# Kernel optimization log

Hardware: AMD Instinct MI355X
Metric: run time of the kernel (lower is better)

Reference implementation:

```python
import jax, jax.numpy as jnp
import numpy as np

EPS = 1e-12
BN_EPS = 1e-5

LAP = jnp.array([[0., 1., 0.], [1., -4., 1.], [0., 1., 0.]], jnp.float32).reshape(1, 1, 3, 3)
SOBX = jnp.array([[-1., 0., 1.], [-2., 0., 2.], [-1., 0., 1.]], jnp.float32).reshape(1, 1, 3, 3)
SOBY = jnp.array([[-1., -2., -1.], [0., 0., 0.], [1., 2., 1.]], jnp.float32).reshape(1, 1, 3, 3)


def _conv3x3(x, w):
    return jax.lax.conv_general_dilated(x, w, (1, 1), 'SAME',
                                        dimension_numbers=('NCHW', 'OIHW', 'NCHW'))


def _bn(x, gamma, beta, mean, var):
    # eval-mode BatchNorm2d with running stats
    inv = gamma / jnp.sqrt(var + BN_EPS)
    return x * inv[None, :, None, None] + (beta - mean * inv)[None, :, None, None]


def _entropy_u8(x01, bins=256):
    # torch.histc(min=0,max=1): bin i = [i/bins,(i+1)/bins), value==1 -> last bin
    B = x01.shape[0]
    flat = jnp.clip(x01, 0.0, 1.0).reshape(B, -1)
    idx = jnp.clip(jnp.floor(flat * bins).astype(jnp.int32), 0, bins - 1)
    h = jnp.zeros((B, bins), flat.dtype).at[jnp.arange(B)[:, None], idx].add(1.0)
    p = h / (h.sum(axis=1, keepdims=True) + EPS)
    safe_p = jnp.where(p > 0, p, 1.0)
    return jnp.where(p > 0, -p * jnp.log2(safe_p), 0.0).sum(axis=1)


def _gini(flat):
    B, N = flat.shape
    xs = jnp.sort(flat, axis=1)
    s = xs.sum(axis=1) + EPS
    w = (N + 1 - jnp.arange(1, N + 1, dtype=flat.dtype))[None, :]
    lor = (w * xs).sum(axis=1) / s
    return (N + 1 - 2.0 * lor) / N


def _grid_cv(E, grid=16):
    B, _, H, W = E.shape  # H,W divisible by grid -> adaptive_avg_pool == block mean
    pooled = E.reshape(B, grid, H // grid, grid, W // grid).mean(axis=(2, 4))
    cells = pooled.reshape(B, -1)
    return cells.std(axis=1) / (cells.mean(axis=1) + EPS)


def _lap_var(x):
    y = _conv3x3(x, LAP)
    return jnp.var(y, axis=(2, 3), ddof=1)[:, 0]  # torch .var default unbiased=True


def _sobel_mean(x):
    gx = _conv3x3(x, SOBX)
    gy = _conv3x3(x, SOBY)
    return jnp.sqrt(gx * gx + gy * gy).mean(axis=(1, 2, 3))


def _colorfulness(R, G, Bc):
    rg = (R - G)[:, 0]
    yb = ((R + G) / 2 - Bc)[:, 0]
    # torch .std default is unbiased (ddof=1)
    s = jnp.sqrt(jnp.std(rg, axis=(1, 2), ddof=1) ** 2 + jnp.std(yb, axis=(1, 2), ddof=1) ** 2)
    m = jnp.sqrt(rg.mean(axis=(1, 2)) ** 2 + yb.mean(axis=(1, 2)) ** 2)
    return s + 0.3 * m


def _metrics(img5):
    B = img5.shape[0]
    P, N = img5[:, 0:1], img5[:, 1:2]
    R, G, Bc = img5[:, 2:3], img5[:, 3:4], img5[:, 4:5]
    Pn, Nn = P / 255.0, N / 255.0
    E = jnp.maximum(Pn + Nn, 0.0)
    Y = jnp.clip(0.299 * R + 0.587 * G + 0.114 * Bc, 0.0, 1.0)
    muY = Y.mean(axis=(1, 2, 3))
    stdY = Y.std(axis=(1, 2, 3))  # unbiased=False
    flatY = Y.reshape(B, -1)
    dr = jnp.quantile(flatY, 0.99, axis=1) - jnp.quantile(flatY, 0.01, axis=1)
    psat = (Y < 0.02).astype(Y.dtype).mean(axis=(1, 2, 3)) + (Y > 0.98).astype(Y.dtype).mean(axis=(1, 2, 3))
    entY = _entropy_u8(Y)
    varlp = _lap_var(Y)
    gmean = _sobel_mean(Y)
    cf = _colorfulness(R, G, Bc)
    nz = (E > 0).astype(E.dtype).mean(axis=(1, 2, 3))
    int_density = E.mean(axis=(1, 2, 3))
    onoff = (Pn.sum(axis=(1, 2, 3)) + EPS) / (Nn.sum(axis=(1, 2, 3)) + EPS)
    gg = _gini(E.reshape(B, -1))
    cvgrid = _grid_cv(E)
    entE = _entropy_u8(E)
    varlpE = _lap_var(E)
    pbias = ((Pn - Nn) / (Pn + Nn + EPS)).mean(axis=(1, 2, 3))
    z16 = jnp.stack([muY, stdY, dr, psat, entY, varlp, gmean, cf, nz, int_density,
                     onoff, gg, cvgrid, entE, varlpE, pbias], axis=1)
    return z16[:, jnp.array([0, 1, 5, 6, 12, 9, 15, 14])]


def _forward(event, frame, conv1_w, bn1_g, bn1_b, bn1_m, bn1_v,
             conv2_w, bn2_g, bn2_b, bn2_m, bn2_v,
             fe_w1, fe_b1, fe_w2, fe_b2, hg_w, hg_b, hf_w, hf_b, res_scale):
    img5 = jnp.concatenate([event, frame], axis=1)  # (B,5,H,W)
    fx = _conv3x3(img5, conv1_w)
    fx = _bn(fx, bn1_g, bn1_b, bn1_m, bn1_v)
    fx = fx * jax.nn.sigmoid(fx)  # SiLU
    fx = _conv3x3(fx, conv2_w)
    fx = _bn(fx, bn2_g, bn2_b, bn2_m, bn2_v)
    z = jax.lax.stop_gradient(_metrics(img5))  # @torch.no_grad()
    h = jax.nn.relu(z @ fe_w1.T + fe_b1)
    h = jax.nn.relu(h @ fe_w2.T + fe_b2)
    g = jax.nn.sigmoid(h @ hg_w.T + hg_b)
    g = g / (g.sum(axis=1, keepdims=True) + EPS)
    film = h @ hf_w.T + hf_b  # (B,10)
    gamma = 1.0 + 0.1 * film[:, :5]
    beta = 0.1 * film[:, 5:]
    fx_film = gamma[:, :, None, None] * fx + beta[:, :, None, None]
    alpha = jnp.concatenate([jnp.repeat(g[:, 0:1], 2, axis=1),
                             jnp.repeat(g[:, 1:2], 3, axis=1)], axis=1)
    fused = fx_film * alpha[:, :, None, None]
    out5 = img5 + res_scale[0] * fused
    return out5


def setup_inputs() -> dict:
    key = jax.random.key(0)
    ks = jax.random.split(key, 21)
    B, H, W = 16, 512, 512
    CH, HID, MD = 16, 64, 8
    u = lambda k, s, off=0.0: jax.random.uniform(k, s, jnp.float32) + off
    n = lambda k, s, sc=0.1: jax.random.normal(k, s, jnp.float32) * sc
    return {
        'event': u(ks[0], (B, 2, H, W)),
        'frame': u(ks[1], (B, 3, H, W)),
        'conv1_w': n(ks[2], (CH, 5, 3, 3)),
        'bn1_g': u(ks[3], (CH,), 0.5), 'bn1_b': n(ks[4], (CH,)),
        'bn1_m': n(ks[5], (CH,)), 'bn1_v': u(ks[6], (CH,), 0.5),
        'conv2_w': n(ks[7], (5, CH, 3, 3)),
        'bn2_g': u(ks[8], (5,), 0.5), 'bn2_b': n(ks[9], (5,)),
        'bn2_m': n(ks[10], (5,)), 'bn2_v': u(ks[11], (5,), 0.5),
        'fe_w1': n(ks[12], (HID, MD)), 'fe_b1': n(ks[13], (HID,)),
        'fe_w2': n(ks[14], (HID, HID)), 'fe_b2': n(ks[15], (HID,)),
        'hg_w': n(ks[16], (2, HID)), 'hg_b': n(ks[17], (2,)),
        'hf_w': n(ks[18], (10, HID)), 'hf_b': n(ks[19], (10,)),
        'res_scale': n(ks[20], (1,)),
    }


def reference(event, frame, conv1_w, bn1_g, bn1_b, bn1_m, bn1_v,
              conv2_w, bn2_g, bn2_b, bn2_m, bn2_v,
              fe_w1, fe_b1, fe_w2, fe_b2, hg_w, hg_b, hf_w, hf_b, res_scale):
    out5 = _forward(event, frame, conv1_w, bn1_g, bn1_b, bn1_m, bn1_v,
                    conv2_w, bn2_g, bn2_b, bn2_m, bn2_v,
                    fe_w1, fe_b1, fe_w2, fe_b2, hg_w, hg_b, hf_w, hf_b, res_scale)
    return out5[:, 0:2], out5[:, 2:5]
```

## Files before the change

### kernel.cpp

```cpp
#include <hip/hip_runtime.h>
#include <hip/hip_bf16.h>

typedef unsigned int   u32;
typedef unsigned short u16;

#define HW 262144
#define W512 512

typedef __attribute__((ext_vector_type(8))) short short8;
typedef __attribute__((ext_vector_type(4))) float f32x4;

__device__ __forceinline__ u32 f2b_rtne(float f) {
    union { float f; u32 i; } c; c.f = f;
    u32 u = c.i;
    return (u + 0x7FFFu + ((u >> 16) & 1u)) >> 16;
}
__device__ __forceinline__ u32 pk_bf16(float lo, float hi) {
    float2 t; t.x = lo; t.y = hi;
    __hip_bfloat162 h = __float22bfloat162_rn(t);
    return *reinterpret_cast<u32*>(&h);
}
__device__ __forceinline__ float lo16(u32 w) {
    union { u32 i; float f; } c; c.i = w << 16; return c.f;
}
__device__ __forceinline__ float hi16(u32 w) {
    union { u32 i; float f; } c; c.i = w & 0xFFFF0000u; return c.f;
}
__device__ __forceinline__ float silu_fast(float v) {
    return v * __builtin_amdgcn_rcpf(1.f + __expf(-v));
}

__device__ __forceinline__ void row6(const u16* rowp, int base, float* o) {
    uint2 A = *reinterpret_cast<const uint2*>(rowp + base - 4);
    uint2 B = *reinterpret_cast<const uint2*>(rowp + base);
    uint2 C = *reinterpret_cast<const uint2*>(rowp + base + 4);
    o[0] = hi16(A.y);
    o[1] = lo16(B.x); o[2] = hi16(B.x);
    o[3] = lo16(B.y); o[4] = hi16(B.y);
    o[5] = lo16(C.x);
}

__global__ __launch_bounds__(1024) void k_band(
    const float* __restrict__ ev, const float* __restrict__ fr,
    int nb, float* __restrict__ partials, float* __restrict__ z)
{
    __shared__ u16 sYb[18][528];
    __shared__ u16 sEb[18][528];
    __shared__ float cellPart[1024];
    __shared__ float cellFull[256];
    __shared__ float red[16][8];

    int blk = blockIdx.x;
    int b = blk / nb, band = blk % nb;
    int rowsPerBand = 512 / nb;
    int chunks = rowsPerBand >> 4;
    int rBase = band * rowsPerBand;
    int tid = threadIdx.x;

    const float* Pp = ev + (size_t)(b * 2)     * HW;
    const float* Np = ev + (size_t)(b * 2 + 1) * HW;
    const float* Rp = fr + (size_t)(b * 3)     * HW;
    const float* Gp = fr + (size_t)(b * 3 + 1) * HW;
    const float* Bp = fr + (size_t)(b * 3 + 2) * HW;

    if (nb == 1 && tid < 256) cellFull[tid] = 0.f;
    if (tid < 36) {
        int rr = tid >> 1, side = tid & 1;
        uint4 zz = {0, 0, 0, 0};
        *reinterpret_cast<uint4*>(&sYb[rr][side ? 520 : 0]) = zz;
        *reinterpret_cast<uint4*>(&sEb[rr][side ? 520 : 0]) = zz;
    }

    float aY = 0, aY2 = 0, aL = 0, aL2 = 0, aG = 0, aPb = 0, aLE = 0, aLE2 = 0;

    for (int ch = 0; ch < chunks; ++ch) {
        int r0 = rBase + ch * 16;
        __syncthreads();
        for (int idx = tid; idx < 2304; idx += 1024) {
            int rl = idx >> 7, q4 = (idx & 127) << 2;
            int gy = r0 - 1 + rl;
            float4 y4 = {0.f, 0.f, 0.f, 0.f};
            float4 e4 = {0.f, 0.f, 0.f, 0.f};
            if (gy >= 0 && gy < W512) {
                size_t o = (size_t)gy * W512 + q4;
                float4 R = *reinterpret_cast<const float4*>(Rp + o);
                float4 G = *reinterpret_cast<const float4*>(Gp + o);
                float4 B = *reinterpret_cast<const float4*>(Bp + o);
                float4 P = *reinterpret_cast<const float4*>(Pp + o);
                float4 N = *reinterpret_cast<const float4*>(Np + o);
                y4.x = fminf(fmaxf(0.299f * R.x + 0.587f * G.x + 0.114f * B.x, 0.f), 1.f);
                y4.y = fminf(fmaxf(0.299f * R.y + 0.587f * G.y + 0.114f * B.y, 0.f), 1.f);
                y4.z = fminf(fmaxf(0.299f * R.z + 0.587f * G.z + 0.114f * B.z, 0.f), 1.f);
                y4.w = fminf(fmaxf(0.299f * R.w + 0.587f * G.w + 0.114f * B.w, 0.f), 1.f);
                e4.x = fmaxf((P.x + N.x) * (1.f / 255.f), 0.f);
                e4.y = fmaxf((P.y + N.y) * (1.f / 255.f), 0.f);
                e4.z = fmaxf((P.z + N.z) * (1.f / 255.f), 0.f);
                e4.w = fmaxf((P.w + N.w) * (1.f / 255.f), 0.f);
                if (rl >= 1 && rl <= 16) {
                    float pnx = P.x * (1.f / 255.f), nnx = N.x * (1.f / 255.f);
                    float pny = P.y * (1.f / 255.f), nny = N.y * (1.f / 255.f);
                    float pnz = P.z * (1.f / 255.f), nnz = N.z * (1.f / 255.f);
                    float pnw = P.w * (1.f / 255.f), nnw = N.w * (1.f / 255.f);
                    aPb += (pnx - nnx) * __builtin_amdgcn_rcpf(pnx + nnx + 1e-12f);
                    aPb += (pny - nny) * __builtin_amdgcn_rcpf(pny + nny + 1e-12f);
                    aPb += (pnz - nnz) * __builtin_amdgcn_rcpf(pnz + nnz + 1e-12f);
                    aPb += (pnw - nnw) * __builtin_amdgcn_rcpf(pnw + nnw + 1e-12f);
                }
            }
            uint2 py, pe;
            py.x = pk_bf16(y4.x, y4.y); py.y = pk_bf16(y4.z, y4.w);
            pe.x = pk_bf16(e4.x, e4.y); pe.y = pk_bf16(e4.z, e4.w);
            *reinterpret_cast<uint2*>(&sYb[rl][8 + q4]) = py;
            *reinterpret_cast<uint2*>(&sEb[rl][8 + q4]) = pe;
        }
        __syncthreads();

        float ce = 0.f;
        #pragma unroll
        for (int q = 0; q < 2; ++q) {
            int qi = tid + (q << 10);
            int row = qi >> 7, c4 = (qi & 127) << 2;
            int lr = row + 1, base = 8 + c4;
            float y0[6], y1[6], y2[6], er[6];
            row6(&sYb[lr - 1][0], base, y0);
            row6(&sYb[lr][0],     base, y1);
            row6(&sYb[lr + 1][0], base, y2);
            row6(&sEb[lr][0],     base, er);
            uint2 U = *reinterpret_cast<const uint2*>(&sEb[lr - 1][base]);
            uint2 D = *reinterpret_cast<const uint2*>(&sEb[lr + 1][base]);
            float eu[4] = {lo16(U.x), hi16(U.x), lo16(U.y), hi16(U.y)};
            float ed[4] = {lo16(D.x), hi16(D.x), lo16(D.y), hi16(D.y)};
            #pragma unroll
            for (int j = 0; j < 4; ++j) {
                float y = y1[j + 1];
                float lap = y0[j + 1] + y2[j + 1] + y1[j] + y1[j + 2] - 4.f * y;
                float gx  = (y0[j + 2] + 2.f * y1[j + 2] + y2[j + 2])
                          - (y0[j]     + 2.f * y1[j]     + y2[j]);
                float gy2 = (y2[j] + 2.f * y2[j + 1] + y2[j + 2])
                          - (y0[j] + 2.f * y0[j + 1] + y0[j + 2]);
                float gm = sqrtf(gx * gx + gy2 * gy2);
                float e = er[j + 1];
                float lapE = eu[j] + ed[j] + er[j] + er[j + 2] - 4.f * e;
                aY += y; aY2 += y * y; aL += lap; aL2 += lap * lap; aG += gm;
                aLE += lapE; aLE2 += lapE * lapE; ce += e;
            }
        }
        cellPart[tid] = ce;
        __syncthreads();
        if (tid < 16) {
            float s = 0.f;
            for (int rg = 0; rg < 8; ++rg)
                for (int k = 0; k < 8; ++k)
                    s += cellPart[rg * 128 + tid * 8 + k];
            if (nb == 1) cellFull[(r0 >> 5) * 16 + tid] += s;
            else         partials[(size_t)blk * 32 + 9 + tid] = s;
        }
    }
    __syncthreads();

    float v[8] = {aY, aY2, aL, aL2, aG, aPb, aLE, aLE2};
    #pragma unroll
    for (int off = 32; off; off >>= 1)
        #pragma unroll
        for (int k = 0; k < 8; ++k) v[k] += __shfl_down(v[k], off);
    int lane = tid & 63, wid = tid >> 6;
    if (lane == 0)
        for (int k = 0; k < 8; ++k) red[wid][k] = v[k];
    __syncthreads();

    if (tid == 0) {
        float s[8];
        for (int k = 0; k < 8; ++k) {
            float t = 0.f;
            for (int w = 0; w < 16; ++w) t += red[w][k];
            s[k] = t;
        }
        if (nb > 1) {
            float* rec = partials + (size_t)blk * 32;
            for (int k = 0; k < 8; ++k) rec[k] = s[k];
        } else {
            float c1 = 0.f, c2 = 0.f, ct = 0.f;
            for (int j = 0; j < 256; ++j) {
                float m = cellFull[j] * (1.f / 1024.f);
                c1 += m; c2 += m * m; ct += cellFull[j];
            }
            const float FN = 262144.f;
            float muY   = s[0] / FN;
            float stdY  = sqrtf(fmaxf(s[1] / FN - muY * muY, 0.f));
            float varlp = fmaxf(s[3] - s[2] * s[2] / FN, 0.f) / (FN - 1.f);
            float gmean = s[4] / FN;
            float mc = c1 * (1.f / 256.f);
            float vc = fmaxf(c2 * (1.f / 256.f) - mc * mc, 0.f);
            float cv = sqrtf(vc) / (mc + 1e-12f);
            float dens = ct / FN;
            float pb = s[5] / FN;
            float varlpE = fmaxf(s[7] - s[6] * s[6] / FN, 0.f) / (FN - 1.f);
            float* zb = z + b * 8;
            zb[0] = muY; zb[1] = stdY; zb[2] = varlp; zb[3] = gmean;
            zb[4] = cv;  zb[5] = dens; zb[6] = pb;    zb[7] = varlpE;
        }
    }
}

__global__ __launch_bounds__(256) void k_finalize(
    const float* __restrict__ partials, float* __restrict__ z)
{
    __shared__ float sred[8];
    __shared__ float rr[4][3];
    int b = blockIdx.x, tid = threadIdx.x;
    if (tid < 8) {
        float s = 0.f;
        for (int band = 0; band < 32; ++band)
            s += partials[(size_t)(b * 32 + band) * 32 + tid];
        sred[tid] = s;
    }
    int cr = tid >> 4, cc = tid & 15;
    float cell = partials[(size_t)(b * 32 + 2 * cr)     * 32 + 9 + cc]
               + partials[(size_t)(b * 32 + 2 * cr + 1) * 32 + 9 + cc];
    float m = cell * (1.f / 1024.f);
    float c1 = m, c2 = m * m, ct = cell;
    #pragma unroll
    for (int off = 32; off; off >>= 1) {
        c1 += __shfl_down(c1, off);
        c2 += __shfl_down(c2, off);
        ct += __shfl_down(ct, off);
    }
    int lane = tid & 63, wid = tid >> 6;
    if (lane == 0) { rr[wid][0] = c1; rr[wid][1] = c2; rr[wid][2] = ct; }
    __syncthreads();
    if (tid == 0) {
        float C1 = rr[0][0] + rr[1][0] + rr[2][0] + rr[3][0];
        float C2 = rr[0][1] + rr[1][1] + rr[2][1] + rr[3][1];
        float CT = rr[0][2] + rr[1][2] + rr[2][2] + rr[3][2];
        const float FN = 262144.f;
        float muY   = sred[0] / FN;
        float stdY  = sqrtf(fmaxf(sred[1] / FN - muY * muY, 0.f));
        float varlp = fmaxf(sred[3] - sred[2] * sred[2] / FN, 0.f) / (FN - 1.f);
        float gmean = sred[4] / FN;
        float mc = C1 * (1.f / 256.f);
        float vc = fmaxf(C2 * (1.f / 256.f) - mc * mc, 0.f);
        float cv = sqrtf(vc) / (mc + 1e-12f);
        float dens = CT / FN;
        float pb = sred[5] / FN;
        float varlpE = fmaxf(sred[7] - sred[6] * sred[6] / FN, 0.f) / (FN - 1.f);
        float* zb = z + b * 8;
        zb[0] = muY; zb[1] = stdY; zb[2] = varlp; zb[3] = gmean;
        zb[4] = cv;  zb[5] = dens; zb[6] = pb;    zb[7] = varlpE;
    }
}

__global__ __launch_bounds__(1024) void k_mlp(
    const float* __restrict__ z,
    const float* __restrict__ w1, const float* __restrict__ b1,
    const float* __restrict__ w2, const float* __restrict__ b2,
    const float* __restrict__ hgw, const float* __restrict__ hgb,
    const float* __restrict__ hfw, const float* __restrict__ hfb,
    const float* __restrict__ rs,
    const float* __restrict__ c1w,
    const float* __restrict__ bn1g, const float* __restrict__ bn1b,
    const float* __restrict__ bn1m, const float* __restrict__ bn1v,
    const float* __restrict__ c2w,
    const float* __restrict__ bn2g, const float* __restrict__ bn2b,
    const float* __restrict__ bn2m, const float* __restrict__ bn2v,
    float* __restrict__ coefA, float* __restrict__ cBp,
    u16* __restrict__ w1frag, u16* __restrict__ w2frag,
    float* __restrict__ b1f)
{
    int j = threadIdx.x, b = threadIdx.y;
    int ft = b * 64 + j;

    for (int t = ft; t < 1536; t += 1024) {
        int m = t >> 9, ln = (t >> 3) & 63, sl = t & 7;
        int oc = ln & 15, gg = ln >> 4;
        int tap = m * 4 + gg;
        float v = 0.f;
        if (tap < 9 && sl < 5)
            v = c1w[oc * 45 + sl * 9 + tap] * (bn1g[oc] * rsqrtf(bn1v[oc] + 1e-5f));
        w1frag[t] = (u16)f2b_rtne(v);
    }
    for (int t = ft; t < 2560; t += 1024) {
        int m = t >> 9, ln = (t >> 3) & 63, sl = t & 7;
        int oc = ln & 15, gg = ln >> 4;
        int tap = 2 * m + (gg >> 1);
        int ic = (gg & 1) * 8 + sl;
        float v = 0.f;
        if (oc < 5 && tap < 9)
            v = c2w[oc * 144 + ic * 9 + tap] * (bn2g[oc] * rsqrtf(bn2v[oc] + 1e-5f));
        w2frag[t] = (u16)f2b_rtne(v);
    }
    if (ft < 16) {
        float inv = bn1g[ft] * rsqrtf(bn1v[ft] + 1e-5f);
        b1f[ft] = bn1b[ft] - bn1m[ft] * inv;
    }

    __shared__ float sZ[16][8], sH1[16][64], sH2[16][64], sG[16][2], sF[16][10];
    if (j < 8) sZ[b][j] = z[b * 8 + j];
    __syncthreads();
    float a = b1[j];
    #pragma unroll
    for (int k = 0; k < 8; ++k) a += sZ[b][k] * w1[j * 8 + k];
    sH1[b][j] = fmaxf(a, 0.f);
    __syncthreads();
    float a2 = b2[j];
    for (int k = 0; k < 64; ++k) a2 += sH1[b][k] * w2[j * 64 + k];
    sH2[b][j] = fmaxf(a2, 0.f);
    __syncthreads();
    if (j < 2) {
        float g = hgb[j];
        for (int k = 0; k < 64; ++k) g += sH2[b][k] * hgw[j * 64 + k];
        sG[b][j] = 1.f / (1.f + __expf(-g));
    }
    if (j < 10) {
        float f = hfb[j];
        for (int k = 0; k < 64; ++k) f += sH2[b][k] * hfw[j * 64 + k];
        sF[b][j] = f;
    }
    __syncthreads();
    if (j < 5) {
        float gs = sG[b][0] + sG[b][1] + 1e-12f;
        float alpha = (j < 2 ? sG[b][0] : sG[b][1]) / gs;
        float gamma = 1.f + 0.1f * sF[b][j];
        float beta  = 0.1f * sF[b][5 + j];
        float r = rs[0];
        float inv2 = bn2g[j] * rsqrtf(bn2v[j] + 1e-5f);
        float b2fold = bn2b[j] - bn2m[j] * inv2;
        float cA = r * alpha * gamma;
        coefA[b * 5 + j] = cA;
        cBp[b * 5 + j]   = r * alpha * beta + cA * b2fold;
    }
}

__global__ __launch_bounds__(256, 4) void k_main(
    const float* __restrict__ ev, const float* __restrict__ fr,
    const u16* __restrict__ w1frag, const u16* __restrict__ w2frag,
    const float* __restrict__ b1f,
    const float* __restrict__ coefA, const float* __restrict__ cBp,
    float* __restrict__ out)
{
    __shared__ __align__(16) u16 sIn[20 * 40 * 8];
    __shared__ __align__(16) u16 sT1[18 * 34 * 16];

    int tid = threadIdx.x;
    int lane = tid & 63, wv = tid >> 6;
    int g = lane >> 4, col = lane & 15;
    int b = blockIdx.z;
    int ty0 = blockIdx.y * 16, tx0 = blockIdx.x * 32;
    bool interior = (blockIdx.x >= 1 && blockIdx.x <= 14 &&
                     blockIdx.y >= 1 && blockIdx.y <= 30);

    const float* p0 = ev + (size_t)(b * 2)     * HW;
    const float* p1 = ev + (size_t)(b * 2 + 1) * HW;
    const float* p2 = fr + (size_t)(b * 3)     * HW;
    const float* p3 = fr + (size_t)(b * 3 + 1) * HW;
    const float* p4 = fr + (size_t)(b * 3 + 2) * HW;

    if (tid < 200) {
        int r = tid / 10, k = tid % 10;
        int gy = ty0 - 2 + r, gx = tx0 - 4 + 4 * k;
        float4 v0, v1, v2, v3, v4;
        if (interior) {
            size_t o = (size_t)gy * W512 + gx;
            v0 = *reinterpret_cast<const float4*>(p0 + o);
            v1 = *reinterpret_cast<const float4*>(p1 + o);
            v2 = *reinterpret_cast<const float4*>(p2 + o);
            v3 = *reinterpret_cast<const float4*>(p3 + o);
            v4 = *reinterpret_cast<const float4*>(p4 + o);
        } else {
            v0 = v1 = v2 = v3 = v4 = float4{0, 0, 0, 0};
            if (gy >= 0 && gy < W512 && gx >= 0 && gx < W512) {
                size_t o = (size_t)gy * W512 + gx;
                v0 = *reinterpret_cast<const float4*>(p0 + o);
                v1 = *reinterpret_cast<const float4*>(p1 + o);
                v2 = *reinterpret_cast<const float4*>(p2 + o);
                v3 = *reinterpret_cast<const float4*>(p3 + o);
                v4 = *reinterpret_cast<const float4*>(p4 + o);
            }
        }
        int base = (r * 40 + 4 * k) * 8;
        const float* a0 = (const float*)&v0;
        const float* a1 = (const float*)&v1;
        const float* a2 = (const float*)&v2;
        const float* a3 = (const float*)&v3;
        const float* a4 = (const float*)&v4;
        #pragma unroll
        for (int jx = 0; jx < 4; ++jx) {
            uint4 pk;
            pk.x = pk_bf16(a0[jx], a1[jx]);
            pk.y = pk_bf16(a2[jx], a3[jx]);
            pk.z = pk_bf16(a4[jx], 0.f);
            pk.w = 0;
            *reinterpret_cast<uint4*>(&sIn[base + jx * 8]) = pk;
        }
    }

    short8 a1f[3], a2f[5];
    #pragma unroll
    for (int m = 0; m < 3; ++m)
        a1f[m] = *reinterpret_cast<const short8*>(&w1frag[(m * 64 + lane) * 8]);
    #pragma unroll
    for (int m = 0; m < 5; ++m)
        a2f[m] = *reinterpret_cast<const short8*>(&w2frag[(m * 64 + lane) * 8]);
    f32x4 b1v = *reinterpret_cast<const f32x4*>(&b1f[g * 4]);

    int boff1[3];
    #pragma unroll
    for (int m = 0; m < 3; ++m) {
        int tap = m * 4 + g; if (tap > 8) tap = 8;
        boff1[m] = ((tap / 3) * 40 + (tap % 3)) * 16;
    }
    int boff2[5];
    #pragma unroll
    for (int m = 0; m < 5; ++m) {
        int tap = 2 * m + (g >> 1); if (tap > 8) tap = 8;
        boff2[m] = ((tap / 3) * 34 + (tap % 3)) * 32 + (g & 1) * 16;
    }

    __syncthreads();

    for (int t = wv; t < 39; t += 8) {
        bool hasB = (t + 4 < 39);
        int qA = t * 16 + col;
        int qB = hasB ? (qA + 64) : qA;
        int qcA = qA > 611 ? 611 : qA;
        int qcB = qB > 611 ? 611 : qB;
        int rA = qcA / 34, cA = qcA - rA * 34;
        int rB = qcB / 34, cB = qcB - rB * 34;
        const char* baseA = (const char*)&sIn[(rA * 40 + cA + 2) * 8];
        const char* baseB = (const char*)&sIn[(rB * 40 + cB + 2) * 8];
        short8 fA0 = *reinterpret_cast<const short8*>(baseA + boff1[0]);
        short8 fB0 = *reinterpret_cast<const short8*>(baseB + boff1[0]);
        short8 fA1 = *reinterpret_cast<const short8*>(baseA + boff1[1]);
        short8 fB1 = *reinterpret_cast<const short8*>(baseB + boff1[1]);
        short8 fA2 = *reinterpret_cast<const short8*>(baseA + boff1[2]);
        short8 fB2 = *reinterpret_cast<const short8*>(baseB + boff1[2]);
        f32x4 accA = b1v;
        f32x4 accB = b1v;
        accA = __builtin_amdgcn_mfma_f32_16x16x32_bf16(a1f[0], fA0, accA, 0, 0, 0);
        accB = __builtin_amdgcn_mfma_f32_16x16x32_bf16(a1f[0], fB0, accB, 0, 0, 0);
        accA = __builtin_amdgcn_mfma_f32_16x16x32_bf16(a1f[1], fA1, accA, 0, 0, 0);
        accB = __builtin_amdgcn_mfma_f32_16x16x32_bf16(a1f[1], fB1, accB, 0, 0, 0);
        accA = __builtin_amdgcn_mfma_f32_16x16x32_bf16(a1f[2], fA2, accA, 0, 0, 0);
        accB = __builtin_amdgcn_mfma_f32_16x16x32_bf16(a1f[2], fB2, accB, 0, 0, 0);

        {
            float v0 = silu_fast(accA[0]);
            float v1 = silu_fast(accA[1]);
            float v2 = silu_fast(accA[2]);
            float v3 = silu_fast(accA[3]);
            if (!interior) {
                int gy1 = ty0 - 1 + rA, gx1 = tx0 - 1 + cA;
                bool inimg = (gy1 >= 0 && gy1 < W512 && gx1 >= 0 && gx1 < W512);
                if (!inimg) { v0 = v1 = v2 = v3 = 0.f; }
            }
            uint2 pk;
            pk.x = pk_bf16(v0, v1);
            pk.y = pk_bf16(v2, v3);
            *reinterpret_cast<uint2*>(&sT1[(rA * 34 + cA) * 16 + g * 4]) = pk;
        }
        if (hasB) {
            float v0 = silu_fast(accB[0]);
            float v1 = silu_fast(accB[1]);
            float v2 = silu_fast(accB[2]);
            float v3 = silu_fast(accB[3]);
            if (!interior) {
                int gy1 = ty0 - 1 + rB, gx1 = tx0 - 1 + cB;
                bool inimg = (gy1 >= 0 && gy1 < W512 && gx1 >= 0 && gx1 < W512);
                if (!inimg) { v0 = v1 = v2 = v3 = 0.f; }
            }
            uint2 pk;
            pk.x = pk_bf16(v0, v1);
            pk.y = pk_bf16(v2, v3);
            *reinterpret_cast<uint2*>(&sT1[(rB * 34 + cB) * 16 + g * 4]) = pk;
        }
    }
    __syncthreads();

    float cA0 = coefA[b * 5 + 0], cA1 = coefA[b * 5 + 1], cA2 = coefA[b * 5 + 2];
    float cA3 = coefA[b * 5 + 3], cA4 = coefA[b * 5 + 4];
    float cB0 = cBp[b * 5 + 0], cB1 = cBp[b * 5 + 1], cB2 = cBp[b * 5 + 2];
    float cB3 = cBp[b * 5 + 3], cB4 = cBp[b * 5 + 4];
    const size_t OUT2 = (size_t)32 * HW;

    for (int t = wv; t < 32; t += 8) {
        int qA = t * 16 + col;
        int qB = qA + 64;
        int rA = qA >> 5, cA = qA & 31;
        int rB = qB >> 5, cB = qB & 31;
        const char* baseA = (const char*)&sT1[(rA * 34 + cA) * 16];
        const char* baseB = (const char*)&sT1[(rB * 34 + cB) * 16];
        f32x4 accA = {0.f, 0.f, 0.f, 0.f};
        f32x4 accB = {0.f, 0.f, 0.f, 0.f};
        #pragma unroll
        for (int m = 0; m < 5; ++m) {
            short8 fA = *reinterpret_cast<const short8*>(baseA + boff2[m]);
            short8 fB = *reinterpret_cast<const short8*>(baseB + boff2[m]);
            accA = __builtin_amdgcn_mfma_f32_16x16x32_bf16(a2f[m], fA, accA, 0, 0, 0);
            accB = __builtin_amdgcn_mfma_f32_16x16x32_bf16(a2f[m], fB, accB, 0, 0, 0);
        }
        size_t pxA = (size_t)(ty0 + rA) * W512 + (tx0 + cA);
        size_t pxB = (size_t)(ty0 + rB) * W512 + (tx0 + cB);
        if (g == 0) {
            out[(size_t)(b * 2 + 0) * HW + pxA] = p0[pxA] + cA0 * accA[0] + cB0;
            out[(size_t)(b * 2 + 0) * HW + pxB] = p0[pxB] + cA0 * accB[0] + cB0;
            out[(size_t)(b * 2 + 1) * HW + pxA] = p1[pxA] + cA1 * accA[1] + cB1;
            out[(size_t)(b * 2 + 1) * HW + pxB] = p1[pxB] + cA1 * accB[1] + cB1;
            out[OUT2 + (size_t)(b * 3 + 0) * HW + pxA] = p2[pxA] + cA2 * accA[2] + cB2;
            out[OUT2 + (size_t)(b * 3 + 0) * HW + pxB] = p2[pxB] + cA2 * accB[2] + cB2;
            out[OUT2 + (size_t)(b * 3 + 1) * HW + pxA] = p3[pxA] + cA3 * accA[3] + cB3;
            out[OUT2 + (size_t)(b * 3 + 1) * HW + pxB] = p3[pxB] + cA3 * accB[3] + cB3;
        } else if (g == 1) {
            out[OUT2 + (size_t)(b * 3 + 2) * HW + pxA] = p4[pxA] + cA4 * accA[0] + cB4;
            out[OUT2 + (size_t)(b * 3 + 2) * HW + pxB] = p4[pxB] + cA4 * accB[0] + cB4;
        }
    }
}

extern "C" void kernel_launch(void* const* d_in, const int* in_sizes, int n_in,
                              void* d_out, int out_size, void* d_ws, size_t ws_size,
                              hipStream_t stream)
{
    const float* ev = (const float*)d_in[0];
    const float* fr = (const float*)d_in[1];

    char* wb = (char*)d_ws;
    float* coefA    = (float*)(wb + 0);
    float* cBp      = (float*)(wb + 320);
    float* b1f      = (float*)(wb + 640);
    u16*   w1frag   = (u16*) (wb + 768);
    u16*   w2frag   = (u16*) (wb + 3840);
    float* zbuf     = (float*)(wb + 8960);
    float* partials = (float*)(wb + 10240);

    bool fast = (ws_size >= 75776);
    int nb   = fast ? 32 : 1;
    int nblk = fast ? 512 : 16;
    k_band<<<dim3(nblk), dim3(1024), 0, stream>>>(ev, fr, nb, partials, zbuf);
    if (fast) k_finalize<<<dim3(16), dim3(256), 0, stream>>>(partials, zbuf);

    k_mlp<<<dim3(1), dim3(64, 16), 0, stream>>>(zbuf,
        (const float*)d_in[12], (const float*)d_in[13], (const float*)d_in[14], (const float*)d_in[15],
        (const float*)d_in[16], (const float*)d_in[17], (const float*)d_in[18], (const float*)d_in[19],
        (const float*)d_in[20],
        (const float*)d_in[2], (const float*)d_in[3], (const float*)d_in[4], (const float*)d_in[5],
        (const float*)d_in[6], (const float*)d_in[7], (const float*)d_in[8], (const float*)d_in[9],
        (const float*)d_in[10], (const float*)d_in[11],
        coefA, cBp, w1frag, w2frag, b1f);

    k_main<<<dim3(16, 32, 16), dim3(256), 0, stream>>>(ev, fr,
        w1frag, w2frag, b1f, coefA, cBp, (float*)d_out);
}
```

Measured before the change: 128.8 us.

## Fold finalize into MLP kernel, widen band stencil per thread, raise k_main occupancy

```diff
diff --git a/kernel.cpp b/kernel.cpp
--- a/kernel.cpp
+++ b/kernel.cpp
@@ -30,14 +30,16 @@
     return v * __builtin_amdgcn_rcpf(1.f + __expf(-v));
 }
 
-__device__ __forceinline__ void row6(const u16* rowp, int base, float* o) {
+__device__ __forceinline__ void unp10(const u16* rowp, int base, float* v) {
     uint2 A = *reinterpret_cast<const uint2*>(rowp + base - 4);
-    uint2 B = *reinterpret_cast<const uint2*>(rowp + base);
-    uint2 C = *reinterpret_cast<const uint2*>(rowp + base + 4);
-    o[0] = hi16(A.y);
-    o[1] = lo16(B.x); o[2] = hi16(B.x);
-    o[3] = lo16(B.y); o[4] = hi16(B.y);
-    o[5] = lo16(C.x);
+    uint4 B = *reinterpret_cast<const uint4*>(rowp + base);
+    uint2 C = *reinterpret_cast<const uint2*>(rowp + base + 8);
+    v[0] = hi16(A.y);
+    v[1] = lo16(B.x); v[2] = hi16(B.x);
+    v[3] = lo16(B.y); v[4] = hi16(B.y);
+    v[5] = lo16(B.z); v[6] = hi16(B.z);
+    v[7] = lo16(B.w); v[8] = hi16(B.w);
+    v[9] = lo16(C.x);
 }
 
 __global__ __launch_bounds__(1024) void k_band(
@@ -116,22 +118,23 @@
         __syncthreads();
 
         float ce = 0.f;
-        #pragma unroll
-        for (int q = 0; q < 2; ++q) {
-            int qi = tid + (q << 10);
-            int row = qi >> 7, c4 = (qi & 127) << 2;
-            int lr = row + 1, base = 8 + c4;
-            float y0[6], y1[6], y2[6], er[6];
-            row6(&sYb[lr - 1][0], base, y0);
-            row6(&sYb[lr][0],     base, y1);
-            row6(&sYb[lr + 1][0], base, y2);
-            row6(&sEb[lr][0],     base, er);
-            uint2 U = *reinterpret_cast<const uint2*>(&sEb[lr - 1][base]);
-            uint2 D = *reinterpret_cast<const uint2*>(&sEb[lr + 1][base]);
-            float eu[4] = {lo16(U.x), hi16(U.x), lo16(U.y), hi16(U.y)};
-            float ed[4] = {lo16(D.x), hi16(D.x), lo16(D.y), hi16(D.y)};
+        {
+            int row = tid >> 6;
+            int c8  = (tid & 63) << 3;
+            int lr = row + 1, base = 8 + c8;
+            float y0[10], y1[10], y2[10], er[10];
+            unp10(&sYb[lr - 1][0], base, y0);
+            unp10(&sYb[lr][0],     base, y1);
+            unp10(&sYb[lr + 1][0], base, y2);
+            unp10(&sEb[lr][0],     base, er);
+            uint4 U = *reinterpret_cast<const uint4*>(&sEb[lr - 1][base]);
+            uint4 D = *reinterpret_cast<const uint4*>(&sEb[lr + 1][base]);
+            float eu[8] = {lo16(U.x), hi16(U.x), lo16(U.y), hi16(U.y),
+                           lo16(U.z), hi16(U.z), lo16(U.w), hi16(U.w)};
+            float ed[8] = {lo16(D.x), hi16(D.x), lo16(D.y), hi16(D.y),
+                           lo16(D.z), hi16(D.z), lo16(D.w), hi16(D.w)};
             #pragma unroll
-            for (int j = 0; j < 4; ++j) {
+            for (int j = 0; j < 8; ++j) {
                 float y = y1[j + 1];
                 float lap = y0[j + 1] + y2[j + 1] + y1[j] + y1[j + 2] - 4.f * y;
                 float gx  = (y0[j + 2] + 2.f * y1[j + 2] + y2[j + 2])
@@ -149,9 +152,9 @@
         __syncthreads();
         if (tid < 16) {
             float s = 0.f;
-            for (int rg = 0; rg < 8; ++rg)
-                for (int k = 0; k < 8; ++k)
-                    s += cellPart[rg * 128 + tid * 8 + k];
+            for (int rg = 0; rg < 16; ++rg)
+                for (int k = 0; k < 4; ++k)
+                    s += cellPart[rg * 64 + tid * 4 + k];
             if (nb == 1) cellFull[(r0 >> 5) * 16 + tid] += s;
             else         partials[(size_t)blk * 32 + 9 + tid] = s;
         }
@@ -202,55 +205,8 @@
     }
 }
 
-__global__ __launch_bounds__(256) void k_finalize(
-    const float* __restrict__ partials, float* __restrict__ z)
-{
-    __shared__ float sred[8];
-    __shared__ float rr[4][3];
-    int b = blockIdx.x, tid = threadIdx.x;
-    if (tid < 8) {
-        float s = 0.f;
-        for (int band = 0; band < 32; ++band)
-            s += partials[(size_t)(b * 32 + band) * 32 + tid];
-        sred[tid] = s;
-    }
-    int cr = tid >> 4, cc = tid & 15;
-    float cell = partials[(size_t)(b * 32 + 2 * cr)     * 32 + 9 + cc]
-               + partials[(size_t)(b * 32 + 2 * cr + 1) * 32 + 9 + cc];
-    float m = cell * (1.f / 1024.f);
-    float c1 = m, c2 = m * m, ct = cell;
-    #pragma unroll
-    for (int off = 32; off; off >>= 1) {
-        c1 += __shfl_down(c1, off);
-        c2 += __shfl_down(c2, off);
-        ct += __shfl_down(ct, off);
-    }
-    int lane = tid & 63, wid = tid >> 6;
-    if (lane == 0) { rr[wid][0] = c1; rr[wid][1] = c2; rr[wid][2] = ct; }
-    __syncthreads();
-    if (tid == 0) {
-        float C1 = rr[0][0] + rr[1][0] + rr[2][0] + rr[3][0];
-        float C2 = rr[0][1] + rr[1][1] + rr[2][1] + rr[3][1];
-        float CT = rr[0][2] + rr[1][2] + rr[2][2] + rr[3][2];
-        const float FN = 262144.f;
-        float muY   = sred[0] / FN;
-        float stdY  = sqrtf(fmaxf(sred[1] / FN - muY * muY, 0.f));
-        float varlp = fmaxf(sred[3] - sred[2] * sred[2] / FN, 0.f) / (FN - 1.f);
-        float gmean = sred[4] / FN;
-        float mc = C1 * (1.f / 256.f);
-        float vc = fmaxf(C2 * (1.f / 256.f) - mc * mc, 0.f);
-        float cv = sqrtf(vc) / (mc + 1e-12f);
-        float dens = CT / FN;
-        float pb = sred[5] / FN;
-        float varlpE = fmaxf(sred[7] - sred[6] * sred[6] / FN, 0.f) / (FN - 1.f);
-        float* zb = z + b * 8;
-        zb[0] = muY; zb[1] = stdY; zb[2] = varlp; zb[3] = gmean;
-        zb[4] = cv;  zb[5] = dens; zb[6] = pb;    zb[7] = varlpE;
-    }
-}
-
 __global__ __launch_bounds__(1024) void k_mlp(
-    const float* __restrict__ z,
+    const float* __restrict__ zbuf, const float* __restrict__ partials, int fast,
     const float* __restrict__ w1, const float* __restrict__ b1,
     const float* __restrict__ w2, const float* __restrict__ b2,
     const float* __restrict__ hgw, const float* __restrict__ hgb,
@@ -293,9 +249,53 @@
         b1f[ft] = bn1b[ft] - bn1m[ft] * inv;
     }
 
-    __shared__ float sZ[16][8], sH1[16][64], sH2[16][64], sG[16][2], sF[16][10];
-    if (j < 8) sZ[b][j] = z[b * 8 + j];
-    __syncthreads();
+    __shared__ float sZ[16][8], sS[16][8], sH1[16][64], sH2[16][64], sG[16][2], sF[16][10];
+
+    if (fast) {
+        if (j < 8) {
+            float s = 0.f;
+            for (int band = 0; band < 32; ++band)
+                s += partials[(size_t)(b * 32 + band) * 32 + j];
+            sS[b][j] = s;
+        }
+        float c1 = 0.f, c2 = 0.f, ct = 0.f;
+        #pragma unroll
+        for (int k = 0; k < 4; ++k) {
+            int idx = j * 4 + k;
+            int cr = idx >> 4, cc = idx & 15;
+            float cell = partials[(size_t)(b * 32 + 2 * cr)     * 32 + 9 + cc]
+                       + partials[(size_t)(b * 32 + 2 * cr + 1) * 32 + 9 + cc];
+            float m = cell * (1.f / 1024.f);
+            c1 += m; c2 += m * m; ct += cell;
+        }
+        #pragma unroll
+        for (int off = 32; off; off >>= 1) {
+            c1 += __shfl_down(c1, off);
+            c2 += __shfl_down(c2, off);
+            ct += __shfl_down(ct, off);
+        }
+        __syncthreads();
+        if (j == 0) {
+            const float FN = 262144.f;
+            float muY   = sS[b][0] / FN;
+            float stdY  = sqrtf(fmaxf(sS[b][1] / FN - muY * muY, 0.f));
+            float varlp = fmaxf(sS[b][3] - sS[b][2] * sS[b][2] / FN, 0.f) / (FN - 1.f);
+            float gmean = sS[b][4] / FN;
+            float mc = c1 * (1.f / 256.f);
+            float vc = fmaxf(c2 * (1.f / 256.f) - mc * mc, 0.f);
+            float cv = sqrtf(vc) / (mc + 1e-12f);
+            float dens = ct / FN;
+            float pb = sS[b][5] / FN;
+            float varlpE = fmaxf(sS[b][7] - sS[b][6] * sS[b][6] / FN, 0.f) / (FN - 1.f);
+            sZ[b][0] = muY; sZ[b][1] = stdY; sZ[b][2] = varlp; sZ[b][3] = gmean;
+            sZ[b][4] = cv;  sZ[b][5] = dens; sZ[b][6] = pb;    sZ[b][7] = varlpE;
+        }
+        __syncthreads();
+    } else {
+        if (j < 8) sZ[b][j] = zbuf[b * 8 + j];
+        __syncthreads();
+    }
+
     float a = b1[j];
     #pragma unroll
     for (int k = 0; k < 8; ++k) a += sZ[b][k] * w1[j * 8 + k];
@@ -330,7 +330,7 @@
     }
 }
 
-__global__ __launch_bounds__(256, 4) void k_main(
+__global__ __launch_bounds__(256, 5) void k_main(
     const float* __restrict__ ev, const float* __restrict__ fr,
     const u16* __restrict__ w1frag, const u16* __restrict__ w2frag,
     const float* __restrict__ b1f,
@@ -535,9 +535,8 @@
     int nb   = fast ? 32 : 1;
     int nblk = fast ? 512 : 16;
     k_band<<<dim3(nblk), dim3(1024), 0, stream>>>(ev, fr, nb, partials, zbuf);
-    if (fast) k_finalize<<<dim3(16), dim3(256), 0, stream>>>(partials, zbuf);
-
-    k_mlp<<<dim3(1), dim3(64, 16), 0, stream>>>(zbuf,
+
+    k_mlp<<<dim3(1), dim3(64, 16), 0, stream>>>(zbuf, partials, fast ? 1 : 0,
         (const float*)d_in[12], (const float*)d_in[13], (const float*)d_in[14], (const float*)d_in[15],
         (const float*)d_in[16], (const float*)d_in[17], (const float*)d_in[18], (const float*)d_in[19],
         (const float*)d_in[20],
```

New measurement: 129.2 us. No clear change (+0.3%).
